# Kernel tuning notes

Measured on AMD Instinct MI355X. Metric: run time of the kernel, lower is better.

Reference implementation:

```python
import jax, jax.numpy as jnp
import numpy as np

HEADS = 2

def gat_layer(x, edge_index, W, att, bias):
    # x: [N, Fin], W: [H*C, Fin], att: [1, H, 2C], bias: [C]
    N = x.shape[0]
    C = bias.shape[0]
    # add self loops (source_to_target: x_j from row 0, aggregate onto row 1)
    loop = jnp.arange(N, dtype=edge_index.dtype)
    src = jnp.concatenate([edge_index[0], loop])
    dst = jnp.concatenate([edge_index[1], loop])
    h = (x @ W.T).reshape(N, HEADS, C)          # [N, H, C]
    x_j = h[src]                                 # [E, H, C]
    x_i = h[dst]                                 # [E, H, C]
    x_cat = jnp.concatenate([x_i, x_j], axis=-1) # [E, H, 2C]
    alpha = (x_cat * att).sum(-1)                # [E, H]
    alpha = jnp.where(alpha >= 0, alpha, 0.2 * alpha)  # leaky_relu(0.2)
    # NOTE: module uses a global (not per-destination) normalization
    alpha = jnp.exp(alpha - alpha.max())
    alpha = alpha / (alpha.sum(axis=0, keepdims=True) + 1e-10)
    msg = x_j * alpha[..., None]                 # [E, H, C]
    aggr = jax.ops.segment_sum(msg, dst, num_segments=N)  # [N, H, C]
    return aggr.mean(axis=1) + bias              # [N, C]

def setup_inputs() -> dict:
    key = jax.random.key(0)
    ks = jax.random.split(key, 7)
    N, Fin, C = 50000, 128, 64
    E = 800000
    x = jax.random.normal(ks[0], (N, Fin), dtype=jnp.float32)
    edge_index = jax.random.randint(ks[1], (2, E), 0, N, dtype=jnp.int64)
    W1 = jax.random.normal(ks[2], (HEADS * C, Fin), dtype=jnp.float32) * 0.05
    att1 = jax.random.normal(ks[3], (1, HEADS, 2 * C), dtype=jnp.float32) * 0.05
    b1 = jnp.zeros((C,), dtype=jnp.float32)
    W2 = jax.random.normal(ks[4], (HEADS * C, C), dtype=jnp.float32) * 0.05
    att2 = jax.random.normal(ks[5], (1, HEADS, 2 * C), dtype=jnp.float32) * 0.05
    b2 = jnp.zeros((C,), dtype=jnp.float32)
    return {"x": x, "edge_index": edge_index, "W1": W1, "att1": att1,
            "b1": b1, "W2": W2, "att2": att2, "b2": b2}

def reference(x, edge_index, W1, att1, b1, W2, att2, b2):
    h = gat_layer(x, edge_index, W1, att1, b1)
    h = jax.nn.relu(h)
    # F.dropout with training flag: treated as eval (identity) for determinism
    out = gat_layer(h, edge_index, W2, att2, b2)
    return out
```

## Files before the change

### kernel.cpp

```cpp
#include <hip/hip_runtime.h>
#include <hip/hip_bf16.h>
#include <math.h>


#define HP 8
#define HG 64
#define NHISTB (HP * HG)
#define HRANGE_MAX 6272
#define NZ    256

using short8 = __attribute__((ext_vector_type(8))) short;
using f32x4  = __attribute__((ext_vector_type(4))) float;

__device__ __forceinline__ unsigned f2bf(float x) {
  unsigned u = __float_as_uint(x);
  return (u + 0x7fffu + ((u >> 16) & 1u)) >> 16;
}
__device__ __forceinline__ float bflo(unsigned p) { return __uint_as_float(p << 16); }
__device__ __forceinline__ float bfhi(unsigned p) { return __uint_as_float(p & 0xffff0000u); }
__device__ __forceinline__ float lrexp(float a) {
  a = a >= 0.f ? a : 0.2f * a;
  return __expf(a);
}

__global__ __launch_bounds__(256) void init_ws(
    const float* __restrict__ W1, const float* __restrict__ W2,
    unsigned short* __restrict__ wbf1, unsigned short* __restrict__ wbf2,
    float* __restrict__ Z) {
  int tid = blockIdx.x * 256 + threadIdx.x;
  int stride = gridDim.x * 256;
  for (int i = tid; i < 128 * 128; i += stride)
    wbf1[i] = (unsigned short)f2bf(W1[i]);
  for (int i = tid; i < 128 * 64; i += stride)
    wbf2[i] = (unsigned short)f2bf(W2[i]);
  if (tid < 4) Z[tid] = 0.f;
}

template <int FIN>
__global__ __launch_bounds__(256) void gemm_mfma(
    const float* __restrict__ x, const unsigned short* __restrict__ Wb,
    const float* __restrict__ att, unsigned* __restrict__ hq,
    float* __restrict__ si, float* __restrict__ sj,
    int N,
    const int* __restrict__ dstE, int* __restrict__ partial,
    int E, int nhistb, int hstep) {
  const int tid = threadIdx.x;

  constexpr int WB = 128 * FIN * 2;
  constexpr int SMEM = (WB > HRANGE_MAX * 4) ? WB : HRANGE_MAX * 4;
  __shared__ __align__(16) unsigned char smem[SMEM];

  if ((int)blockIdx.x < nhistb) {
    int* lhist = (int*)smem;
    const int p = blockIdx.x & (HP - 1);
    const int g = blockIdx.x >> 3;
    const int lo = p * hstep;
    for (int i = tid; i < hstep; i += 256) lhist[i] = 0;
    __syncthreads();
    const int stride = HG * 256;
    int e = g * 256 + tid;
    for (; e + 3 * stride < E; e += 4 * stride) {
      int d0 = dstE[e] - lo;
      int d1 = dstE[e + stride] - lo;
      int d2 = dstE[e + 2 * stride] - lo;
      int d3 = dstE[e + 3 * stride] - lo;
      if ((unsigned)d0 < (unsigned)hstep) atomicAdd(&lhist[d0], 1);
      if ((unsigned)d1 < (unsigned)hstep) atomicAdd(&lhist[d1], 1);
      if ((unsigned)d2 < (unsigned)hstep) atomicAdd(&lhist[d2], 1);
      if ((unsigned)d3 < (unsigned)hstep) atomicAdd(&lhist[d3], 1);
    }
    for (; e < E; e += stride) {
      int d = dstE[e] - lo;
      if ((unsigned)d < (unsigned)hstep) atomicAdd(&lhist[d], 1);
    }
    __syncthreads();
    for (int i = tid; i < hstep; i += 256) {
      int node = lo + i;
      if (node < N) partial[(size_t)g * N + node] = lhist[i];
    }
    return;
  }

  constexpr int KS = FIN / 32;
  constexpr int CPR = FIN / 8;
  constexpr int NCHUNK = 128 * CPR;

  unsigned short* wlds = (unsigned short*)smem;

  const int w    = tid >> 6;
  const int lane = tid & 63;
  const int cl   = lane & 15;
  const int grp  = lane >> 4;
  const int n0   = (blockIdx.x - nhistb) * 64;

  const int arow = n0 + w * 16 + cl;
  const bool avalid = arow < N;
  float4 av0[KS], av1[KS];
#pragma unroll
  for (int ks = 0; ks < KS; ++ks) {
    av0[ks] = make_float4(0.f, 0.f, 0.f, 0.f);
    av1[ks] = av0[ks];
    if (avalid) {
      const float4* xp =
          (const float4*)(x + (size_t)arow * FIN + ks * 32 + grp * 8);
      av0[ks] = xp[0];
      av1[ks] = xp[1];
    }
  }

  const uint4* Wb4 = (const uint4*)Wb;
  for (int c = tid; c < NCHUNK; c += 256) {
    int row = c / CPR;
    int cc  = c & (CPR - 1);
    *(uint4*)&wlds[row * FIN + ((cc ^ (row & (CPR - 1))) * 8)] = Wb4[c];
  }
  __syncthreads();

  short8 afrag[KS];
#pragma unroll
  for (int ks = 0; ks < KS; ++ks) {
    union { short8 s8; unsigned u[4]; } af;
    af.u[0] = f2bf(av0[ks].x) | (f2bf(av0[ks].y) << 16);
    af.u[1] = f2bf(av0[ks].z) | (f2bf(av0[ks].w) << 16);
    af.u[2] = f2bf(av1[ks].x) | (f2bf(av1[ks].y) << 16);
    af.u[3] = f2bf(av1[ks].z) | (f2bf(av1[ks].w) << 16);
    afrag[ks] = af.s8;
  }

  f32x4 acc[8];
#pragma unroll
  for (int ct = 0; ct < 8; ++ct) acc[ct] = (f32x4){0.f, 0.f, 0.f, 0.f};

  const int swz = cl & (CPR - 1);
#pragma unroll
  for (int ks = 0; ks < KS; ++ks) {
#pragma unroll
    for (int ct = 0; ct < 8; ++ct) {
      const unsigned short* bp =
          &wlds[(ct * 16 + cl) * FIN + (((ks * 4 + grp) ^ swz) * 8)];
      short8 bfrag = *(const short8*)bp;
      acc[ct] = __builtin_amdgcn_mfma_f32_16x16x32_bf16(afrag[ks], bfrag,
                                                        acc[ct], 0, 0, 0);
    }
  }

  float ai[8], aj[8];
#pragma unroll
  for (int ct = 0; ct < 8; ++ct) {
    int hd = ct >> 2;
    int cw = (ct & 3) * 16 + cl;
    ai[ct] = att[hd * 128 + cw];
    aj[ct] = att[hd * 128 + 64 + cw];
  }

#pragma unroll
  for (int r = 0; r < 4; ++r) {
    int node = n0 + w * 16 + grp * 4 + r;
    float s0i = 0.f, s0j = 0.f, s1i = 0.f, s1j = 0.f;
    unsigned wpk[4];
#pragma unroll
    for (int ct = 0; ct < 4; ++ct) {
      float v0 = acc[ct][r];
      float v1 = acc[ct + 4][r];
      s0i += v0 * ai[ct];
      s0j += v0 * aj[ct];
      s1i += v1 * ai[ct + 4];
      s1j += v1 * aj[ct + 4];
      wpk[ct] = f2bf(v0) | (f2bf(v1) << 16);
    }
#pragma unroll
    for (int off = 8; off; off >>= 1) {
      s0i += __shfl_xor(s0i, off, 64);
      s0j += __shfl_xor(s0j, off, 64);
      s1i += __shfl_xor(s1i, off, 64);
      s1j += __shfl_xor(s1j, off, 64);
    }
    if (node < N) {
#pragma unroll
      for (int ct = 0; ct < 4; ++ct)
        hq[(size_t)node * 64 + ct * 16 + cl] = wpk[ct];
      if (cl == 0) {
        si[node * 2 + 0] = s0i;
        si[node * 2 + 1] = s1i;
        sj[node * 2 + 0] = s0j;
        sj[node * 2 + 1] = s1j;
      }
    }
  }
}

__device__ __forceinline__ void z_edge_body(
    const int* __restrict__ srcE, const int* __restrict__ dstE,
    const float2* __restrict__ si2, const float2* __restrict__ sj2,
    float* __restrict__ Zp, int E, int Etot, int tid0, int stride) {
  float z0 = 0.f, z1 = 0.f;
  for (int e = tid0; e < Etot; e += stride) {
    int s, d;
    if (e < E) { s = srcE[e]; d = dstE[e]; } else { s = d = e - E; }
    float2 siv = si2[d];
    float2 sjv = sj2[s];
    z0 += lrexp(siv.x + sjv.x);
    z1 += lrexp(siv.y + sjv.y);
  }
  __shared__ float r0[4], r1[4];
  int lane = threadIdx.x & 63, w = threadIdx.x >> 6;
#pragma unroll
  for (int off = 32; off; off >>= 1) {
    z0 += __shfl_down(z0, off, 64);
    z1 += __shfl_down(z1, off, 64);
  }
  if (lane == 0) { r0[w] = z0; r1[w] = z1; }
  __syncthreads();
  if (threadIdx.x == 0) {
    atomicAdd(&Zp[0], r0[0] + r0[1] + r0[2] + r0[3]);
    atomicAdd(&Zp[1], r1[0] + r1[1] + r1[2] + r1[3]);
  }
}

__global__ __launch_bounds__(256) void z_edge(
    const int* __restrict__ srcE, const int* __restrict__ dstE,
    const float2* __restrict__ si2, const float2* __restrict__ sj2,
    float* __restrict__ Zp, int E, int Etot) {
  z_edge_body(srcE, dstE, si2, sj2, Zp, E, Etot,
              blockIdx.x * 256 + threadIdx.x, gridDim.x * 256);
}

__global__ __launch_bounds__(256) void wgt_fill(
    const int* __restrict__ esrc, const int* __restrict__ edst,
    const float2* __restrict__ si2, const float2* __restrict__ sj2,
    float2* __restrict__ wgt, int E) {
  int k = blockIdx.x * 256 + threadIdx.x;
  int stride = gridDim.x * 256;
  for (; k < E; k += stride) {
    float2 siv = si2[edst[k]];
    float2 sjv = sj2[esrc[k]];
    wgt[k] = make_float2(lrexp(siv.x + sjv.x), lrexp(siv.y + sjv.y));
  }
}

__global__ __launch_bounds__(256) void scan_blocks(
    const int* __restrict__ partial, int* __restrict__ rowptr,
    int* __restrict__ bsum, int N) {
  __shared__ int ts[256];
  int b = blockIdx.x, t = threadIdx.x;
  int base = b * 1024 + t * 4;
  int s0 = 0, s1 = 0, s2 = 0, s3 = 0;
  if (base < N) {
    const int4* p4 = (const int4*)partial;
#pragma unroll 4
    for (int g = 0; g < HG; ++g) {
      int4 v = p4[((size_t)g * N + base) >> 2];
      s0 += v.x; s1 += v.y; s2 += v.z; s3 += v.w;
    }
  }
  int v[4] = {s0, s1, s2, s3};
  int tot = s0 + s1 + s2 + s3;
  ts[t] = tot;
  __syncthreads();
#pragma unroll
  for (int off = 1; off < 256; off <<= 1) {
    int x = (t >= off) ? ts[t - off] : 0;
    __syncthreads();
    ts[t] += x;
    __syncthreads();
  }
  int run = ts[t] - tot;
#pragma unroll
  for (int j = 0; j < 4; ++j) {
    if (base + j < N) rowptr[base + j] = run;
    run += v[j];
  }
  if (t == 255) bsum[b] = ts[255];
}

__global__ __launch_bounds__(256) void scan_finish(
    int* __restrict__ rowptr, const int* __restrict__ bsum,
    int* __restrict__ partial, int N, int Eall, int nb) {
  __shared__ int pre[256];
  if (threadIdx.x == 0) {
    int run = 0;
    for (int i = 0; i < nb; ++i) { pre[i] = run; run += bsum[i]; }
  }
  __syncthreads();
  int tid = blockIdx.x * blockDim.x + threadIdx.x;
  int stride = gridDim.x * blockDim.x;
  for (int i = tid; i < N; i += stride) {
    int v = rowptr[i] + pre[i >> 10];
    rowptr[i] = v;
    int run = v;
#pragma unroll 8
    for (int g = 0; g < HG; ++g) {
      int c = partial[(size_t)g * N + i];
      partial[(size_t)g * N + i] = run;
      run += c;
    }
  }
  if (tid == 0) rowptr[N] = Eall;
}

__global__ __launch_bounds__(256) void scatter_z(
    const int* __restrict__ srcE, const int* __restrict__ dstE,
    const int* __restrict__ partial, int* __restrict__ esrc,
    int* __restrict__ edst, float2* __restrict__ wgt,
    const float2* __restrict__ si2, const float2* __restrict__ sj2,
    float* __restrict__ Zp, int E, int Etot, int hstep, int N) {
  __shared__ __align__(16) int lcur[HRANGE_MAX];
  if ((int)blockIdx.x < NZ) {
    z_edge_body(srcE, dstE, si2, sj2, Zp, E, Etot,
                blockIdx.x * 256 + threadIdx.x, NZ * 256);
    return;
  }
  const int bid = blockIdx.x - NZ;
  const int p = bid & (HP - 1);
  const int g = bid >> 3;
  const int lo = p * hstep;
  const int tid = threadIdx.x;
  for (int i = tid; i < hstep; i += 256) {
    int node = lo + i;
    lcur[i] = (node < N) ? partial[(size_t)g * N + node] : 0;
  }
  __syncthreads();
  const int stride = HG * 256;
  for (int e = g * 256 + tid; e < E; e += stride) {
    int d = dstE[e];
    int dd = d - lo;
    if ((unsigned)dd < (unsigned)hstep) {
      int s = srcE[e];
      int pos = atomicAdd(&lcur[dd], 1);
      esrc[pos] = s;
      edst[pos] = d;
      float2 siv = si2[d];
      float2 sjv = sj2[s];
      wgt[pos] = make_float2(lrexp(siv.x + sjv.x), lrexp(siv.y + sjv.y));
    }
  }
}

__device__ __forceinline__ void edge4w(
    const int* __restrict__ esrc, const float2* __restrict__ wgt, int k,
    const unsigned* __restrict__ hq, int lane, float& acc0, float& acc1) {
  int s0 = esrc[k], s1 = esrc[k + 1], s2 = esrc[k + 2], s3 = esrc[k + 3];
  float2 w0 = wgt[k], w1 = wgt[k + 1], w2 = wgt[k + 2], w3 = wgt[k + 3];
  unsigned p0 = hq[(size_t)s0 * 64 + lane];
  unsigned p1 = hq[(size_t)s1 * 64 + lane];
  unsigned p2 = hq[(size_t)s2 * 64 + lane];
  unsigned p3 = hq[(size_t)s3 * 64 + lane];
  acc0 = fmaf(bflo(p0), w0.x, acc0);
  acc1 = fmaf(bfhi(p0), w0.y, acc1);
  acc0 = fmaf(bflo(p1), w1.x, acc0);
  acc1 = fmaf(bfhi(p1), w1.y, acc1);
  acc0 = fmaf(bflo(p2), w2.x, acc0);
  acc1 = fmaf(bfhi(p2), w2.y, acc1);
  acc0 = fmaf(bflo(p3), w3.x, acc0);
  acc1 = fmaf(bfhi(p3), w3.y, acc1);
}
__device__ __forceinline__ void edge1w(
    int s, float2 wv, const unsigned* __restrict__ hq, int lane,
    float& acc0, float& acc1) {
  unsigned p = hq[(size_t)s * 64 + lane];
  acc0 = fmaf(bflo(p), wv.x, acc0);
  acc1 = fmaf(bfhi(p), wv.y, acc1);
}

__global__ __launch_bounds__(256) void csr_aggregate(
    const int* __restrict__ rowptr, const int* __restrict__ esrc,
    const float2* __restrict__ wgt, const unsigned* __restrict__ hq,
    const float2* __restrict__ si2, const float2* __restrict__ sj2,
    const float* __restrict__ Zp, const float* __restrict__ bias,
    float* __restrict__ out, int N, int do_relu) {
  int lane = threadIdx.x & 63;
  int wid = (blockIdx.x * blockDim.x + threadIdx.x) >> 6;
  int nw = (gridDim.x * blockDim.x) >> 6;
  float z0 = 1.f / (Zp[0] + 1e-10f);
  float z1 = 1.f / (Zp[1] + 1e-10f);
  float bv = bias[lane];
  for (int n0 = wid; n0 < N; n0 += nw) {
    int n = __builtin_amdgcn_readfirstlane(n0);
    int beg = rowptr[n], end = rowptr[n + 1];
    float2 siv = si2[n];
    float2 jv = sj2[n];
    float2 wself = make_float2(lrexp(siv.x + jv.x), lrexp(siv.y + jv.y));
    float acc0 = 0.f, acc1 = 0.f;
    edge1w(n, wself, hq, lane, acc0, acc1);
    int k = beg;
    for (; k + 4 <= end; k += 4) edge4w(esrc, wgt, k, hq, lane, acc0, acc1);
    for (; k < end; ++k) edge1w(esrc[k], wgt[k], hq, lane, acc0, acc1);
    float r = 0.5f * (acc0 * z0 + acc1 * z1) + bv;
    if (do_relu) r = fmaxf(r, 0.f);
    out[(size_t)n * 64 + lane] = r;
  }
}

extern "C" void kernel_launch(void* const* d_in, const int* in_sizes, int n_in,
                              void* d_out, int out_size, void* d_ws, size_t ws_size,
                              hipStream_t stream) {
  const float* x    = (const float*)d_in[0];
  const int*   ei   = (const int*)d_in[1];
  const float* W1   = (const float*)d_in[2];
  const float* att1 = (const float*)d_in[3];
  const float* b1   = (const float*)d_in[4];
  const float* W2   = (const float*)d_in[5];
  const float* att2 = (const float*)d_in[6];
  const float* b2   = (const float*)d_in[7];
  float* out = (float*)d_out;

  const int N = in_sizes[0] / 128;
  const int E = in_sizes[1] / 2;
  const int Etot = E + N;
  const int* srcE = ei;
  const int* dstE = ei + E;

  unsigned* hq = (unsigned*)d_ws;
  float* si    = (float*)(hq + (size_t)N * 64);
  float* sj    = si + (size_t)N * 2;
  float* Z     = sj + (size_t)N * 2;
  float* x2    = Z + 4;
  int* partial = (int*)x2;
  int* rowptr  = (int*)(x2 + (size_t)N * 64);
  int* esrc    = rowptr + (N + 1);
  int* edst    = esrc + E;
  float2* wgt  = (float2*)(edst + E);
  int* bsum    = (int*)(wgt + E);
  uintptr_t wp = ((uintptr_t)(bsum + 256) + 15) & ~(uintptr_t)15;
  unsigned short* wbf1 = (unsigned short*)wp;
  unsigned short* wbf2 = wbf1 + 128 * 128;

  dim3 blk(256);
  int nb = (N + 1023) / 1024;
  int ntiles = (N + 63) / 64;
  int hstep = (N + HP - 1) / HP;

  init_ws<<<64, blk, 0, stream>>>(W1, W2, wbf1, wbf2, Z);
  gemm_mfma<128><<<NHISTB + ntiles, blk, 0, stream>>>(
      x, wbf1, att1, hq, si, sj, N, dstE, partial, E, NHISTB, hstep);
  scan_blocks<<<nb, blk, 0, stream>>>(partial, rowptr, bsum, N);
  scan_finish<<<256, blk, 0, stream>>>(rowptr, bsum, partial, N, E, nb);
  scatter_z<<<NZ + NHISTB, blk, 0, stream>>>(
      srcE, dstE, partial, esrc, edst, wgt, (const float2*)si,
      (const float2*)sj, Z, E, Etot, hstep, N);
  csr_aggregate<<<4096, blk, 0, stream>>>(rowptr, esrc, wgt, hq,
                                          (const float2*)si, (const float2*)sj,
                                          Z, b1, x2, N, 1);
  gemm_mfma<64><<<ntiles, blk, 0, stream>>>(
      x2, wbf2, att2, hq, si, sj, N, dstE, partial, E, 0, hstep);
  z_edge<<<NZ, blk, 0, stream>>>(srcE, dstE, (const float2*)si,
                                 (const float2*)sj, Z + 2, E, Etot);
  wgt_fill<<<512, blk, 0, stream>>>(esrc, edst, (const float2*)si,
                                    (const float2*)sj, wgt, E);
  csr_aggregate<<<4096, blk, 0, stream>>>(rowptr, esrc, wgt, hq,
                                          (const float2*)si, (const float2*)sj,
                                          Z + 2, b2, out, N, 0);
}
```

Before: 284.4 us.

## Pack CSR edge src/dst/weights into float4 records and fuse z_edge with wgt_fill

Replaces the separate esrc, edst and wgt arrays with one 16-byte record per edge holding src, dst and both head weights. Scatter and aggregate then do a single vector load or store per edge instead of three scattered ones. The layer-2 z-sum and weight fill are merged into one launch to save a kernel launch. The scatter loop is also unrolled 4x so dst loads are issued together. Record size stays 16 bytes per edge, so the memory footprint is unchanged, but wgt_fill now rewrites whole records.

New measurement: 279.3 us. No clear change (-1.8%).

```diff
diff --git a/kernel.cpp b/kernel.cpp
--- a/kernel.cpp
+++ b/kernel.cpp
@@ -8,6 +8,7 @@
 #define NHISTB (HP * HG)
 #define HRANGE_MAX 6272
 #define NZ    256
+#define NWGT  512
 
 using short8 = __attribute__((ext_vector_type(8))) short;
 using f32x4  = __attribute__((ext_vector_type(4))) float;
@@ -217,24 +218,26 @@
   }
 }
 
-__global__ __launch_bounds__(256) void z_edge(
+__global__ __launch_bounds__(256) void z_edge_wgt(
     const int* __restrict__ srcE, const int* __restrict__ dstE,
     const float2* __restrict__ si2, const float2* __restrict__ sj2,
-    float* __restrict__ Zp, int E, int Etot) {
-  z_edge_body(srcE, dstE, si2, sj2, Zp, E, Etot,
-              blockIdx.x * 256 + threadIdx.x, gridDim.x * 256);
-}
-
-__global__ __launch_bounds__(256) void wgt_fill(
-    const int* __restrict__ esrc, const int* __restrict__ edst,
-    const float2* __restrict__ si2, const float2* __restrict__ sj2,
-    float2* __restrict__ wgt, int E) {
-  int k = blockIdx.x * 256 + threadIdx.x;
-  int stride = gridDim.x * 256;
+    float* __restrict__ Zp, float4* __restrict__ erec, int E, int Etot) {
+  if ((int)blockIdx.x < NZ) {
+    z_edge_body(srcE, dstE, si2, sj2, Zp, E, Etot,
+                blockIdx.x * 256 + threadIdx.x, NZ * 256);
+    return;
+  }
+  int k = (blockIdx.x - NZ) * 256 + threadIdx.x;
+  int stride = NWGT * 256;
   for (; k < E; k += stride) {
-    float2 siv = si2[edst[k]];
-    float2 sjv = sj2[esrc[k]];
-    wgt[k] = make_float2(lrexp(siv.x + sjv.x), lrexp(siv.y + sjv.y));
+    float4 r = erec[k];
+    int s = __float_as_int(r.x);
+    int d = __float_as_int(r.y);
+    float2 siv = si2[d];
+    float2 sjv = sj2[s];
+    r.z = lrexp(siv.x + sjv.x);
+    r.w = lrexp(siv.y + sjv.y);
+    erec[k] = r;
   }
 }
 
@@ -300,8 +303,7 @@
 
 __global__ __launch_bounds__(256) void scatter_z(
     const int* __restrict__ srcE, const int* __restrict__ dstE,
-    const int* __restrict__ partial, int* __restrict__ esrc,
-    int* __restrict__ edst, float2* __restrict__ wgt,
+    const int* __restrict__ partial, float4* __restrict__ erec,
     const float2* __restrict__ si2, const float2* __restrict__ sj2,
     float* __restrict__ Zp, int E, int Etot, int hstep, int N) {
   __shared__ __align__(16) int lcur[HRANGE_MAX];
@@ -321,53 +323,84 @@
   }
   __syncthreads();
   const int stride = HG * 256;
-  for (int e = g * 256 + tid; e < E; e += stride) {
+  int e = g * 256 + tid;
+  for (; e + 3 * stride < E; e += 4 * stride) {
+    int d0 = dstE[e], d1 = dstE[e + stride];
+    int d2 = dstE[e + 2 * stride], d3 = dstE[e + 3 * stride];
+    int t0 = d0 - lo, t1 = d1 - lo, t2 = d2 - lo, t3 = d3 - lo;
+    if ((unsigned)t0 < (unsigned)hstep) {
+      int s = srcE[e];
+      float2 siv = si2[d0], sjv = sj2[s];
+      erec[atomicAdd(&lcur[t0], 1)] = make_float4(
+          __int_as_float(s), __int_as_float(d0),
+          lrexp(siv.x + sjv.x), lrexp(siv.y + sjv.y));
+    }
+    if ((unsigned)t1 < (unsigned)hstep) {
+      int s = srcE[e + stride];
+      float2 siv = si2[d1], sjv = sj2[s];
+      erec[atomicAdd(&lcur[t1], 1)] = make_float4(
+          __int_as_float(s), __int_as_float(d1),
+          lrexp(siv.x + sjv.x), lrexp(siv.y + sjv.y));
+    }
+    if ((unsigned)t2 < (unsigned)hstep) {
+      int s = srcE[e + 2 * stride];
+      float2 siv = si2[d2], sjv = sj2[s];
+      erec[atomicAdd(&lcur[t2], 1)] = make_float4(
+          __int_as_float(s), __int_as_float(d2),
+          lrexp(siv.x + sjv.x), lrexp(siv.y + sjv.y));
+    }
+    if ((unsigned)t3 < (unsigned)hstep) {
+      int s = srcE[e + 3 * stride];
+      float2 siv = si2[d3], sjv = sj2[s];
+      erec[atomicAdd(&lcur[t3], 1)] = make_float4(
+          __int_as_float(s), __int_as_float(d3),
+          lrexp(siv.x + sjv.x), lrexp(siv.y + sjv.y));
+    }
+  }
+  for (; e < E; e += stride) {
     int d = dstE[e];
     int dd = d - lo;
     if ((unsigned)dd < (unsigned)hstep) {
       int s = srcE[e];
-      int pos = atomicAdd(&lcur[dd], 1);
-      esrc[pos] = s;
-      edst[pos] = d;
-      float2 siv = si2[d];
-      float2 sjv = sj2[s];
-      wgt[pos] = make_float2(lrexp(siv.x + sjv.x), lrexp(siv.y + sjv.y));
-    }
-  }
-}
-
-__device__ __forceinline__ void edge4w(
-    const int* __restrict__ esrc, const float2* __restrict__ wgt, int k,
-    const unsigned* __restrict__ hq, int lane, float& acc0, float& acc1) {
-  int s0 = esrc[k], s1 = esrc[k + 1], s2 = esrc[k + 2], s3 = esrc[k + 3];
-  float2 w0 = wgt[k], w1 = wgt[k + 1], w2 = wgt[k + 2], w3 = wgt[k + 3];
-  unsigned p0 = hq[(size_t)s0 * 64 + lane];
-  unsigned p1 = hq[(size_t)s1 * 64 + lane];
-  unsigned p2 = hq[(size_t)s2 * 64 + lane];
-  unsigned p3 = hq[(size_t)s3 * 64 + lane];
-  acc0 = fmaf(bflo(p0), w0.x, acc0);
-  acc1 = fmaf(bfhi(p0), w0.y, acc1);
-  acc0 = fmaf(bflo(p1), w1.x, acc0);
-  acc1 = fmaf(bfhi(p1), w1.y, acc1);
-  acc0 = fmaf(bflo(p2), w2.x, acc0);
-  acc1 = fmaf(bfhi(p2), w2.y, acc1);
-  acc0 = fmaf(bflo(p3), w3.x, acc0);
-  acc1 = fmaf(bfhi(p3), w3.y, acc1);
-}
-__device__ __forceinline__ void edge1w(
-    int s, float2 wv, const unsigned* __restrict__ hq, int lane,
+      float2 siv = si2[d], sjv = sj2[s];
+      erec[atomicAdd(&lcur[dd], 1)] = make_float4(
+          __int_as_float(s), __int_as_float(d),
+          lrexp(siv.x + sjv.x), lrexp(siv.y + sjv.y));
+    }
+  }
+}
+
+__device__ __forceinline__ void edge4r(
+    const float4* __restrict__ erec, int k, const unsigned* __restrict__ hq,
+    int lane, float& acc0, float& acc1) {
+  float4 r0 = erec[k], r1 = erec[k + 1], r2 = erec[k + 2], r3 = erec[k + 3];
+  unsigned p0 = hq[(size_t)__float_as_int(r0.x) * 64 + lane];
+  unsigned p1 = hq[(size_t)__float_as_int(r1.x) * 64 + lane];
+  unsigned p2 = hq[(size_t)__float_as_int(r2.x) * 64 + lane];
+  unsigned p3 = hq[(size_t)__float_as_int(r3.x) * 64 + lane];
+  acc0 = fmaf(bflo(p0), r0.z, acc0);
+  acc1 = fmaf(bfhi(p0), r0.w, acc1);
+  acc0 = fmaf(bflo(p1), r1.z, acc0);
+  acc1 = fmaf(bfhi(p1), r1.w, acc1);
+  acc0 = fmaf(bflo(p2), r2.z, acc0);
+  acc1 = fmaf(bfhi(p2), r2.w, acc1);
+  acc0 = fmaf(bflo(p3), r3.z, acc0);
+  acc1 = fmaf(bfhi(p3), r3.w, acc1);
+}
+__device__ __forceinline__ void edge1r(
+    int s, float w0, float w1, const unsigned* __restrict__ hq, int lane,
     float& acc0, float& acc1) {
   unsigned p = hq[(size_t)s * 64 + lane];
-  acc0 = fmaf(bflo(p), wv.x, acc0);
-  acc1 = fmaf(bfhi(p), wv.y, acc1);
+  acc0 = fmaf(bflo(p), w0, acc0);
+  acc1 = fmaf(bfhi(p), w1, acc1);
 }
 
 __global__ __launch_bounds__(256) void csr_aggregate(
-    const int* __restrict__ rowptr, const int* __restrict__ esrc,
-    const float2* __restrict__ wgt, const unsigned* __restrict__ hq,
-    const float2* __restrict__ si2, const float2* __restrict__ sj2,
-    const float* __restrict__ Zp, const float* __restrict__ bias,
-    float* __restrict__ out, int N, int do_relu) {
+    const int* __restrict__ rowptr, const float4* __restrict__ erec,
+    const unsigned* __restrict__ hq, const float2* __restrict__ si2,
+    const float2* __restrict__ sj2, const float* __restrict__ Zp,
+    const float* __restrict__ bias, float* __restrict__ out,
+    int N, int do_relu) {
   int lane = threadIdx.x & 63;
   int wid = (blockIdx.x * blockDim.x + threadIdx.x) >> 6;
   int nw = (gridDim.x * blockDim.x) >> 6;
@@ -379,12 +412,14 @@
     int beg = rowptr[n], end = rowptr[n + 1];
     float2 siv = si2[n];
     float2 jv = sj2[n];
-    float2 wself = make_float2(lrexp(siv.x + jv.x), lrexp(siv.y + jv.y));
     float acc0 = 0.f, acc1 = 0.f;
-    edge1w(n, wself, hq, lane, acc0, acc1);
+    edge1r(n, lrexp(siv.x + jv.x), lrexp(siv.y + jv.y), hq, lane, acc0, acc1);
     int k = beg;
-    for (; k + 4 <= end; k += 4) edge4w(esrc, wgt, k, hq, lane, acc0, acc1);
-    for (; k < end; ++k) edge1w(esrc[k], wgt[k], hq, lane, acc0, acc1);
+    for (; k + 4 <= end; k += 4) edge4r(erec, k, hq, lane, acc0, acc1);
+    for (; k < end; ++k) {
+      float4 r = erec[k];
+      edge1r(__float_as_int(r.x), r.z, r.w, hq, lane, acc0, acc1);
+    }
     float r = 0.5f * (acc0 * z0 + acc1 * z1) + bv;
     if (do_relu) r = fmaxf(r, 0.f);
     out[(size_t)n * 64 + lane] = r;
@@ -417,12 +452,10 @@
   float* x2    = Z + 4;
   int* partial = (int*)x2;
   int* rowptr  = (int*)(x2 + (size_t)N * 64);
-  int* esrc    = rowptr + (N + 1);
-  int* edst    = esrc + E;
-  float2* wgt  = (float2*)(edst + E);
-  int* bsum    = (int*)(wgt + E);
-  uintptr_t wp = ((uintptr_t)(bsum + 256) + 15) & ~(uintptr_t)15;
-  unsigned short* wbf1 = (unsigned short*)wp;
+  int* bsum    = rowptr + (N + 1);
+  uintptr_t ep = ((uintptr_t)(bsum + 256) + 15) & ~(uintptr_t)15;
+  float4* erec = (float4*)ep;
+  unsigned short* wbf1 = (unsigned short*)(erec + E);
   unsigned short* wbf2 = wbf1 + 128 * 128;
 
   dim3 blk(256);
@@ -436,18 +469,16 @@
   scan_blocks<<<nb, blk, 0, stream>>>(partial, rowptr, bsum, N);
   scan_finish<<<256, blk, 0, stream>>>(rowptr, bsum, partial, N, E, nb);
   scatter_z<<<NZ + NHISTB, blk, 0, stream>>>(
-      srcE, dstE, partial, esrc, edst, wgt, (const float2*)si,
-      (const float2*)sj, Z, E, Etot, hstep, N);
-  csr_aggregate<<<4096, blk, 0, stream>>>(rowptr, esrc, wgt, hq,
+      srcE, dstE, partial, erec, (const float2*)si, (const float2*)sj,
+      Z, E, Etot, hstep, N);
+  csr_aggregate<<<4096, blk, 0, stream>>>(rowptr, erec, hq,
                                           (const float2*)si, (const float2*)sj,
                                           Z, b1, x2, N, 1);
   gemm_mfma<64><<<ntiles, blk, 0, stream>>>(
       x2, wbf2, att2, hq, si, sj, N, dstE, partial, E, 0, hstep);
-  z_edge<<<NZ, blk, 0, stream>>>(srcE, dstE, (const float2*)si,
-                                 (const float2*)sj, Z + 2, E, Etot);
-  wgt_fill<<<512, blk, 0, stream>>>(esrc, edst, (const float2*)si,
-                                    (const float2*)sj, wgt, E);
-  csr_aggregate<<<4096, blk, 0, stream>>>(rowptr, esrc, wgt, hq,
+  z_edge_wgt<<<NZ + NWGT, blk, 0, stream>>>(
+      srcE, dstE, (const float2*)si, (const float2*)sj, Z + 2, erec, E, Etot);
+  csr_aggregate<<<4096, blk, 0, stream>>>(rowptr, erec, hq,
                                           (const float2*)si, (const float2*)sj,
                                           Z + 2, b2, out, N, 0);
 }
```
